# Kernel tuning notes

Measured on AMD Instinct MI355X. Metric: run time of the kernel, lower is better.

## Reference

```python
import jax, jax.numpy as jnp
import numpy as np

V, E, H, B, T, O = 100000, 300, 512, 512, 64, 2


def setup_inputs() -> dict:
    key = jax.random.key(0)
    ks = jax.random.split(key, 12)
    bound = 1.0 / np.sqrt(H)
    u = lambda k, shape: jax.random.uniform(k, shape, jnp.float32, -bound, bound)
    tokens = jax.random.randint(ks[0], (B, T), 0, V)  # int token ids
    emb = jax.random.normal(ks[1], (V, E), jnp.float32) * 0.05  # pretrained embeddings
    # GRU params stacked over 2 directions: [2, 3H, in], [2, 3H, H], [2, 3H]
    w_ih0 = u(ks[2], (2, 3 * H, E))
    w_hh0 = u(ks[3], (2, 3 * H, H))
    b_ih0 = u(ks[4], (2, 3 * H))
    b_hh0 = u(ks[5], (2, 3 * H))
    w_ih1 = u(ks[6], (2, 3 * H, 2 * H))
    w_hh1 = u(ks[7], (2, 3 * H, H))
    b_ih1 = u(ks[8], (2, 3 * H))
    b_hh1 = u(ks[9], (2, 3 * H))
    fc_w = u(ks[10], (O, 2 * H))
    fc_b = u(ks[11], (O,))
    return dict(tokens=tokens, emb=emb, w_ih0=w_ih0, w_hh0=w_hh0, b_ih0=b_ih0,
                b_hh0=b_hh0, w_ih1=w_ih1, w_hh1=w_hh1, b_ih1=b_ih1, b_hh1=b_hh1,
                fc_w=fc_w, fc_b=fc_b)


def _gru_dir(x, Wih, Whh, bih, bhh):
    # x: [B, T, in] -> [B, T, H]; PyTorch GRU cell math.
    gx = jnp.einsum('bti,gi->btg', x, Wih) + bih  # input gates precomputed [B,T,3H]
    h_units = Whh.shape[1]

    def step(h, g):
        gh = h @ Whh.T + bhh
        xr, xz, xn = jnp.split(g, 3, axis=-1)
        hr, hz, hn = jnp.split(gh, 3, axis=-1)
        r = jax.nn.sigmoid(xr + hr)
        z = jax.nn.sigmoid(xz + hz)
        n = jnp.tanh(xn + r * hn)
        h_new = (1.0 - z) * n + z * h
        return h_new, h_new

    h0 = jnp.zeros((x.shape[0], h_units), x.dtype)
    _, ys = jax.lax.scan(step, h0, jnp.swapaxes(gx, 0, 1))  # scan over time
    return jnp.swapaxes(ys, 0, 1)


def _gru_bidir(x, w_ih, w_hh, b_ih, b_hh):
    fwd = _gru_dir(x, w_ih[0], w_hh[0], b_ih[0], b_hh[0])
    bwd = _gru_dir(x[:, ::-1], w_ih[1], w_hh[1], b_ih[1], b_hh[1])[:, ::-1]
    return jnp.concatenate([fwd, bwd], axis=-1)  # [B, T, 2H]


def reference(tokens, emb, w_ih0, w_hh0, b_ih0, b_hh0, w_ih1, w_hh1, b_ih1,
              b_hh1, fc_w, fc_b):
    x = emb[tokens]                                   # [B, T, E]
    h1 = _gru_bidir(x, w_ih0, w_hh0, b_ih0, b_hh0)    # [B, T, 2H]
    h2 = _gru_bidir(h1, w_ih1, w_hh1, b_ih1, b_hh1)   # [B, T, 2H]
    # dropout output is discarded in the original forward (out = output[:, -1, :])
    last = h2[:, -1, :]                               # [B, 2H]
    return last @ fc_w.T + fc_b                       # [B, O]
```

## Files before the change

### kernel.cpp

```cpp
#include <hip/hip_runtime.h>
#include <stdint.h>


#define NTW 192
#define MTX 2048

typedef _Float16 half8 __attribute__((ext_vector_type(8)));
typedef _Float16 half4_t __attribute__((ext_vector_type(4)));
typedef float float4_t __attribute__((ext_vector_type(4)));

__device__ __forceinline__ void gl_lds16(const void* g, void* l) {
  __builtin_amdgcn_global_load_lds(
      (const __attribute__((address_space(1))) void*)g,
      (__attribute__((address_space(3))) void*)l, 16, 0, 0);
}

__device__ __forceinline__ float sigm_f(float x) { return 1.f / (1.f + __expf(-x)); }
__device__ __forceinline__ float tanh_f(float x) { return 1.f - 2.f / (__expf(2.f * x) + 1.f); }

__global__ void pack_b_kernel(const float* __restrict__ src, _Float16* __restrict__ dst,
                              int K, int KI) {
  int gid = blockIdx.x * 256 + threadIdx.x;
  int l = gid & 63, unit = gid >> 6;
  int nt = unit / KI, ks = unit - nt * KI;
  if (nt >= NTW) return;
  int row = nt * 16 + (l & 15);
  int col0 = ks * 32 + ((l >> 4) << 3);
  half8 v;
#pragma unroll
  for (int j = 0; j < 8; ++j) {
    int c = col0 + j;
    v[j] = (c < K) ? (_Float16)src[(long)row * K + c] : (_Float16)0.f;
  }
  *(half8*)(dst + (long)unit * 512 + l * 8) = v;
}

__global__ void gather_kernel(const int* __restrict__ tokens, const float* __restrict__ emb,
                              _Float16* __restrict__ x0) {
  int gid = blockIdx.x * 256 + threadIdx.x;
  int l = gid & 63, unit = gid >> 6;
  int mt = unit / 10, ks = unit - mt * 10;
  if (mt >= MTX) return;
  int row = mt * 16 + (l & 15);
  const float* e = emb + (long)tokens[row] * 300;
  int col0 = ks * 32 + ((l >> 4) << 3);
  half8 v;
#pragma unroll
  for (int j = 0; j < 8; ++j) {
    int c = col0 + j;
    v[j] = (c < 300) ? (_Float16)e[c] : (_Float16)0.f;
  }
  *(half8*)(x0 + (long)unit * 512 + l * 8) = v;
}

__global__ __launch_bounds__(256) void gemm_bt_kernel(
    const _Float16* __restrict__ A, const _Float16* __restrict__ Bw,
    const float* __restrict__ bias, _Float16* __restrict__ C, int KI) {
  __shared__ _Float16 As[8 * 512];
  __shared__ _Float16 Bs[8 * 512];
  const int bx = blockIdx.x, by = blockIdx.y;
  const int tid = threadIdx.x, w = tid >> 6, l = tid & 63;
  const int wm = w >> 1, wn = w & 1, ln = l & 15;
  const int mt0 = by * 8, nt0 = bx * 8;
  float4_t acc[4][4];
#pragma unroll
  for (int i = 0; i < 4; ++i)
#pragma unroll
    for (int j = 0; j < 4; ++j) acc[i][j] = 0.f;
  for (int it = 0; it < KI; ++it) {
    __syncthreads();
    gl_lds16(A + ((long)(mt0 + w) * KI + it) * 512 + l * 8, As + w * 512 + l * 8);
    gl_lds16(A + ((long)(mt0 + w + 4) * KI + it) * 512 + l * 8, As + (w + 4) * 512 + l * 8);
    gl_lds16(Bw + ((long)(nt0 + w) * KI + it) * 512 + l * 8, Bs + w * 512 + l * 8);
    gl_lds16(Bw + ((long)(nt0 + w + 4) * KI + it) * 512 + l * 8, Bs + (w + 4) * 512 + l * 8);
    __syncthreads();
    half8 af[4], bf[4];
#pragma unroll
    for (int i = 0; i < 4; ++i) af[i] = *(const half8*)(As + (wm * 4 + i) * 512 + l * 8);
#pragma unroll
    for (int j = 0; j < 4; ++j) bf[j] = *(const half8*)(Bs + (wn * 4 + j) * 512 + l * 8);
#pragma unroll
    for (int i = 0; i < 4; ++i)
#pragma unroll
      for (int j = 0; j < 4; ++j)
        acc[i][j] = __builtin_amdgcn_mfma_f32_16x16x32_f16(af[i], bf[j], acc[i][j], 0, 0, 0);
  }
#pragma unroll
  for (int i = 0; i < 4; ++i)
#pragma unroll
    for (int j = 0; j < 4; ++j) {
      int mt = mt0 + wm * 4 + i, ntile = nt0 + wn * 4 + j;
      float bv = bias[ntile * 16 + ln];
      half4_t o;
#pragma unroll
      for (int r = 0; r < 4; ++r) o[r] = (_Float16)(acc[i][j][r] + bv);
      *(half4_t*)(C + ((long)mt * NTW + ntile) * 256 + l * 4) = o;
    }
}

__global__ __launch_bounds__(256, 1) void gru_scan_kernel(
    const _Float16* __restrict__ whh,
    const float* __restrict__ bhh,
    const _Float16* __restrict__ gx,
    _Float16* hbuf, _Float16* ys,
    float* last,
    unsigned int* cnt) {
  __shared__ alignas(16) _Float16 hsA[16 * 512];
  __shared__ alignas(16) _Float16 hsB[16 * 512];
  __shared__ alignas(16) _Float16 hx[2 * 512];
  const int bid = blockIdx.x;
  const int d = bid >> 7, mp = (bid >> 3) & 15, ntb = bid & 7;
  const int rA = mp * 2, rB = rA + 1;
  const int tid = threadIdx.x, w = tid >> 6, l = tid & 63;
  const int lq = l >> 4, ln = l & 15;
  unsigned int* flagsA = cnt + (d * 32 + rA) * 16;
  unsigned int* flagsB = cnt + (d * 32 + rB) * 16;
  const int hcol = ntb * 64 + w * 16 + ln;

  half8 bf[3][16];
#pragma unroll
  for (int g = 0; g < 3; ++g) {
    const int tg = d * 96 + g * 32 + ntb * 4 + w;
#pragma unroll
    for (int ks = 0; ks < 16; ++ks)
      bf[g][ks] = *(const half8*)(whh + (long)(tg * 16 + ks) * 512 + l * 8);
  }
  const float bh0 = bhh[d * 1536 + hcol];
  const float bh1 = bhh[d * 1536 + 512 + hcol];
  const float bh2 = bhh[d * 1536 + 1024 + hcol];
  float hrA[4] = {0.f, 0.f, 0.f, 0.f};
  float hrB[4] = {0.f, 0.f, 0.f, 0.f};
  const int ntg0 = d * 96 + ntb * 4 + w;
  const unsigned long long* hb8 = (const unsigned long long*)hbuf;
  unsigned long long* hb8w = (unsigned long long*)hbuf;
  unsigned long long* lA64 = (unsigned long long*)hsA;
  unsigned long long* lB64 = (unsigned long long*)hsB;
  const unsigned long long* hx64 = (const unsigned long long*)hx;

  float xrA[4], xzA[4], xnA[4], xrB[4], xzB[4], xnB[4];
  auto load_gx = [&](int step, int rc, float (&vr)[4], float (&vz)[4], float (&vn)[4]) {
    const int t2 = d ? (63 - step) : step;
    const int rm2 = t2 & 15, tq2 = t2 >> 4;
    const int eoff2 = ((rm2 >> 2) * 16 + ln) * 4 + (rm2 & 3);
#pragma unroll
    for (int r = 0; r < 4; ++r) {
      const int b = rc * 16 + lq * 4 + r;
      const long gbase = ((long)(b * 4 + tq2) * 192 + ntg0) * 256 + eoff2;
      vr[r] = (float)gx[gbase];
      vz[r] = (float)gx[gbase + 32 * 256];
      vn[r] = (float)gx[gbase + 64 * 256];
    }
  };
  load_gx(0, rA, xrA, xzA, xnA);
  load_gx(0, rB, xrB, xzB, xnB);

  auto poll = [&](unsigned int* flags, unsigned int tgt) {
    long guard = 0;
    for (;;) {
      const unsigned int f = __hip_atomic_load(flags + (l & 7), __ATOMIC_RELAXED,
                                               __HIP_MEMORY_SCOPE_AGENT);
      if (__all((int)(f >= tgt))) break;
      __builtin_amdgcn_s_sleep(1);
      if (++guard > (1L << 24)) break;
    }
  };

  for (int s = 0; s < 64; ++s) {
    const int par = s & 1;
    const int t_in = d ? (63 - s) : s;
    const int rm = t_in & 15, tq = t_in >> 4;
    const unsigned long long* src = hb8 + (long)(d * 2 + par) * 65536;

    poll(flagsA, (unsigned int)s);
    poll(flagsB, (unsigned int)s);
    __builtin_amdgcn_fence(__ATOMIC_ACQUIRE, "workgroup");
    unsigned long long ta[8], tb[8];
#pragma unroll
    for (int j = 0; j < 8; ++j)
      ta[j] = __hip_atomic_load(src + (long)rA * 2048 + j * 256 + tid, __ATOMIC_RELAXED,
                                __HIP_MEMORY_SCOPE_AGENT);
#pragma unroll
    for (int j = 0; j < 8; ++j)
      tb[j] = __hip_atomic_load(src + (long)rB * 2048 + j * 256 + tid, __ATOMIC_RELAXED,
                                __HIP_MEMORY_SCOPE_AGENT);
#pragma unroll
    for (int j = 0; j < 8; ++j) lA64[j * 256 + tid] = ta[j];
    __syncthreads();

    float4_t accA[3];
    accA[0] = 0.f; accA[1] = 0.f; accA[2] = 0.f;
#pragma unroll
    for (int kk = 0; kk < 2; ++kk) {
      half8 af[8];
#pragma unroll
      for (int k2 = 0; k2 < 8; ++k2)
        af[k2] = *(const half8*)(hsA + (kk * 8 + k2) * 512 + l * 8);
#pragma unroll
      for (int k2 = 0; k2 < 8; ++k2)
#pragma unroll
        for (int g = 0; g < 3; ++g)
          accA[g] = __builtin_amdgcn_mfma_f32_16x16x32_f16(af[k2], bf[g][kk * 8 + k2],
                                                           accA[g], 0, 0, 0);
    }
#pragma unroll
    for (int j = 0; j < 8; ++j) lB64[j * 256 + tid] = tb[j];

#pragma unroll
    for (int r = 0; r < 4; ++r) {
      const int b = rA * 16 + lq * 4 + r;
      const long gmt = (long)b * 4 + tq;
      const float rg = sigm_f(xrA[r] + accA[0][r] + bh0);
      const float zg = sigm_f(xzA[r] + accA[1][r] + bh1);
      const float ng = tanh_f(xnA[r] + rg * (accA[2][r] + bh2));
      const float hv = (1.f - zg) * ng + zg * hrA[r];
      hrA[r] = hv;
      hx[(w >> 1) * 512 + (((w & 1) * 2 + (ln >> 3)) * 16 + lq * 4 + r) * 8 + (ln & 7)] =
          (_Float16)hv;
      if (ys != nullptr) {
        const int kcol = d * 512 + hcol;
        ys[(gmt * 32 + (kcol >> 5)) * 512 + (((kcol >> 3) & 3) * 16 + rm) * 8 + (kcol & 7)] =
            (_Float16)hv;
      }
      if (last != nullptr && ((d == 0 && s == 63) || (d == 1 && s == 0)))
        last[(long)b * 1024 + d * 512 + hcol] = hv;
    }
    __syncthreads();

    if (s < 63) {
      const unsigned long long qa = hx64[tid];
      unsigned long long* dst = hb8w + (long)(d * 2 + (par ^ 1)) * 65536 +
                                (long)rA * 2048 + (ntb * 2 + (tid >> 7)) * 128 + (tid & 127);
      __hip_atomic_store(dst, qa, __ATOMIC_RELAXED, __HIP_MEMORY_SCOPE_AGENT);
    }

    float4_t accB[3];
    accB[0] = 0.f; accB[1] = 0.f; accB[2] = 0.f;
#pragma unroll
    for (int kk = 0; kk < 2; ++kk) {
      half8 af[8];
#pragma unroll
      for (int k2 = 0; k2 < 8; ++k2)
        af[k2] = *(const half8*)(hsB + (kk * 8 + k2) * 512 + l * 8);
#pragma unroll
      for (int k2 = 0; k2 < 8; ++k2)
#pragma unroll
        for (int g = 0; g < 3; ++g)
          accB[g] = __builtin_amdgcn_mfma_f32_16x16x32_f16(af[k2], bf[g][kk * 8 + k2],
                                                           accB[g], 0, 0, 0);
    }
    __syncthreads();
    if (tid == 0 && s < 63)
      __hip_atomic_store(flagsA + ntb, (unsigned int)(s + 1), __ATOMIC_RELAXED,
                         __HIP_MEMORY_SCOPE_AGENT);

#pragma unroll
    for (int r = 0; r < 4; ++r) {
      const int b = rB * 16 + lq * 4 + r;
      const long gmt = (long)b * 4 + tq;
      const float rg = sigm_f(xrB[r] + accB[0][r] + bh0);
      const float zg = sigm_f(xzB[r] + accB[1][r] + bh1);
      const float ng = tanh_f(xnB[r] + rg * (accB[2][r] + bh2));
      const float hv = (1.f - zg) * ng + zg * hrB[r];
      hrB[r] = hv;
      hx[(w >> 1) * 512 + (((w & 1) * 2 + (ln >> 3)) * 16 + lq * 4 + r) * 8 + (ln & 7)] =
          (_Float16)hv;
      if (ys != nullptr) {
        const int kcol = d * 512 + hcol;
        ys[(gmt * 32 + (kcol >> 5)) * 512 + (((kcol >> 3) & 3) * 16 + rm) * 8 + (kcol & 7)] =
            (_Float16)hv;
      }
      if (last != nullptr && ((d == 0 && s == 63) || (d == 1 && s == 0)))
        last[(long)b * 1024 + d * 512 + hcol] = hv;
    }
    if (s == 63) break;

    __syncthreads();
    {
      const unsigned long long qb = hx64[tid];
      unsigned long long* dst = hb8w + (long)(d * 2 + (par ^ 1)) * 65536 +
                                (long)rB * 2048 + (ntb * 2 + (tid >> 7)) * 128 + (tid & 127);
      __hip_atomic_store(dst, qb, __ATOMIC_RELAXED, __HIP_MEMORY_SCOPE_AGENT);
    }
    __syncthreads();
    if (tid == 0)
      __hip_atomic_store(flagsB + ntb, (unsigned int)(s + 1), __ATOMIC_RELAXED,
                         __HIP_MEMORY_SCOPE_AGENT);

    load_gx(s + 1, rA, xrA, xzA, xnA);
    load_gx(s + 1, rB, xrB, xzB, xnB);
  }
}

__global__ void fc_kernel(const float* __restrict__ lastb, const float* __restrict__ fw,
                          const float* __restrict__ fb, float* __restrict__ out) {
  const int b = blockIdx.x, l = threadIdx.x;
  const float* x = lastb + (long)b * 1024;
  float a0 = 0.f, a1 = 0.f;
  for (int k = l; k < 1024; k += 64) {
    const float v = x[k];
    a0 += v * fw[k];
    a1 += v * fw[1024 + k];
  }
#pragma unroll
  for (int off = 32; off > 0; off >>= 1) {
    a0 += __shfl_down(a0, off, 64);
    a1 += __shfl_down(a1, off, 64);
  }
  if (l == 0) {
    out[b * 2 + 0] = a0 + fb[0];
    out[b * 2 + 1] = a1 + fb[1];
  }
}

extern "C" void kernel_launch(void* const* d_in, const int* in_sizes, int n_in,
                              void* d_out, int out_size, void* d_ws, size_t ws_size,
                              hipStream_t stream) {
  const int* tokens = (const int*)d_in[0];
  const float* emb = (const float*)d_in[1];
  const float* w_ih0 = (const float*)d_in[2];
  const float* w_hh0 = (const float*)d_in[3];
  const float* b_ih0 = (const float*)d_in[4];
  const float* b_hh0 = (const float*)d_in[5];
  const float* w_ih1 = (const float*)d_in[6];
  const float* w_hh1 = (const float*)d_in[7];
  const float* b_ih1 = (const float*)d_in[8];
  const float* b_hh1 = (const float*)d_in[9];
  const float* fc_w = (const float*)d_in[10];
  const float* fc_b = (const float*)d_in[11];
  float* out = (float*)d_out;

  char* ws = (char*)d_ws;
  size_t off = 0;
  auto alloc = [&](size_t bytes) -> void* {
    void* p = ws + off;
    off += (bytes + 255) & ~(size_t)255;
    return p;
  };
  _Float16* W0f = (_Float16*)alloc(192L * 10 * 512 * 2);
  _Float16* W1f = (_Float16*)alloc(192L * 32 * 512 * 2);
  _Float16* Wh0f = (_Float16*)alloc(192L * 16 * 512 * 2);
  _Float16* Wh1f = (_Float16*)alloc(192L * 16 * 512 * 2);
  _Float16* x0f = (_Float16*)alloc(2048L * 10 * 512 * 2);
  _Float16* x1f = (_Float16*)alloc(2048L * 32 * 512 * 2);
  _Float16* gxb = (_Float16*)alloc(2048L * 192 * 256 * 2);
  char* hz = ws + off;
  _Float16* hbuf = (_Float16*)alloc(4L * 32 * 8192 * 2);
  unsigned int* cnt = (unsigned int*)alloc(4096);
  const size_t hz_bytes = 4L * 32 * 8192 * 2 + 4096;
  float* lastb = (float*)alloc(512L * 1024 * 4);
  if (off > ws_size) return;

  pack_b_kernel<<<dim3(192 * 10 * 64 / 256), 256, 0, stream>>>(w_ih0, W0f, 300, 10);
  pack_b_kernel<<<dim3(192 * 32 * 64 / 256), 256, 0, stream>>>(w_ih1, W1f, 1024, 32);
  pack_b_kernel<<<dim3(192 * 16 * 64 / 256), 256, 0, stream>>>(w_hh0, Wh0f, 512, 16);
  pack_b_kernel<<<dim3(192 * 16 * 64 / 256), 256, 0, stream>>>(w_hh1, Wh1f, 512, 16);
  gather_kernel<<<dim3(2048 * 10 * 64 / 256), 256, 0, stream>>>(tokens, emb, x0f);

  gemm_bt_kernel<<<dim3(24, 256), 256, 0, stream>>>(x0f, W0f, b_ih0, gxb, 10);
  hipMemsetAsync(hz, 0, hz_bytes, stream);
  gru_scan_kernel<<<dim3(256), 256, 0, stream>>>(Wh0f, b_hh0, gxb, hbuf, x1f, nullptr, cnt);

  gemm_bt_kernel<<<dim3(24, 256), 256, 0, stream>>>(x1f, W1f, b_ih1, gxb, 32);
  hipMemsetAsync(hz, 0, hz_bytes, stream);
  gru_scan_kernel<<<dim3(256), 256, 0, stream>>>(Wh1f, b_hh1, gxb, hbuf, nullptr, lastb, cnt);

  fc_kernel<<<dim3(512), 64, 0, stream>>>(lastb, fc_w, fc_b, out);
}
```

Measured before the change: 1.218 ms.

## Replace flag counters with sentinel-valued per-step hidden-state slots for inter-block sync

The scan kernel stops publishing per-row flag counters and polling them before reading the hidden state. Instead each time step gets its own buffer slot, pre-filled with an all-ones sentinel, and consumers spin directly on the data until no word equals the sentinel. This removes the flag round trip and the extra barriers around flag stores. Row-B polling is also deferred until after the row-A MFMA work so the two waits can overlap. The cost is a much larger hidden-state buffer (64 slots per direction) that must be memset to the sentinel before each layer, adding memset traffic. It also assumes a real fp16 hidden-state word never equals the sentinel, and replaces __syncthreads with a hand-written lgkmcnt wait plus s_barrier.

Measured after the change: 1.398 ms. 1.15x slower.

```diff
diff --git a/kernel.cpp b/kernel.cpp
--- a/kernel.cpp
+++ b/kernel.cpp
@@ -17,6 +17,12 @@
 
 __device__ __forceinline__ float sigm_f(float x) { return 1.f / (1.f + __expf(-x)); }
 __device__ __forceinline__ float tanh_f(float x) { return 1.f - 2.f / (__expf(2.f * x) + 1.f); }
+
+__device__ __forceinline__ void ldsbar() {
+  asm volatile("s_waitcnt lgkmcnt(0)" ::: "memory");
+  __builtin_amdgcn_sched_barrier(0);
+  __builtin_amdgcn_s_barrier();
+}
 
 __global__ void pack_b_kernel(const float* __restrict__ src, _Float16* __restrict__ dst,
                               int K, int KI) {
@@ -103,8 +109,7 @@
     const float* __restrict__ bhh,
     const _Float16* __restrict__ gx,
     _Float16* hbuf, _Float16* ys,
-    float* last,
-    unsigned int* cnt) {
+    float* last) {
   __shared__ alignas(16) _Float16 hsA[16 * 512];
   __shared__ alignas(16) _Float16 hsB[16 * 512];
   __shared__ alignas(16) _Float16 hx[2 * 512];
@@ -113,8 +118,6 @@
   const int rA = mp * 2, rB = rA + 1;
   const int tid = threadIdx.x, w = tid >> 6, l = tid & 63;
   const int lq = l >> 4, ln = l & 15;
-  unsigned int* flagsA = cnt + (d * 32 + rA) * 16;
-  unsigned int* flagsB = cnt + (d * 32 + rB) * 16;
   const int hcol = ntb * 64 + w * 16 + ln;
 
   half8 bf[3][16];
@@ -136,6 +139,7 @@
   unsigned long long* lA64 = (unsigned long long*)hsA;
   unsigned long long* lB64 = (unsigned long long*)hsB;
   const unsigned long long* hx64 = (const unsigned long long*)hx;
+  const unsigned long long SENT = ~0ULL;
 
   float xrA[4], xzA[4], xnA[4], xrB[4], xzB[4], xnB[4];
   auto load_gx = [&](int step, int rc, float (&vr)[4], float (&vz)[4], float (&vn)[4]) {
@@ -154,38 +158,33 @@
   load_gx(0, rA, xrA, xzA, xnA);
   load_gx(0, rB, xrB, xzB, xnB);
 
-  auto poll = [&](unsigned int* flags, unsigned int tgt) {
-    long guard = 0;
-    for (;;) {
-      const unsigned int f = __hip_atomic_load(flags + (l & 7), __ATOMIC_RELAXED,
-                                               __HIP_MEMORY_SCOPE_AGENT);
-      if (__all((int)(f >= tgt))) break;
-      __builtin_amdgcn_s_sleep(1);
-      if (++guard > (1L << 24)) break;
+  auto poll8 = [&](const unsigned long long* src, unsigned long long (&t)[8]) {
+#pragma unroll
+    for (int j = 0; j < 8; ++j)
+      t[j] = __hip_atomic_load(src + j * 256 + tid, __ATOMIC_RELAXED,
+                               __HIP_MEMORY_SCOPE_AGENT);
+#pragma unroll
+    for (int j = 0; j < 8; ++j) {
+      long guard = 0;
+      while (t[j] == SENT) {
+        __builtin_amdgcn_s_sleep(1);
+        t[j] = __hip_atomic_load(src + j * 256 + tid, __ATOMIC_RELAXED,
+                                 __HIP_MEMORY_SCOPE_AGENT);
+        if (++guard > (1L << 24)) break;
+      }
     }
   };
 
   for (int s = 0; s < 64; ++s) {
-    const int par = s & 1;
     const int t_in = d ? (63 - s) : s;
     const int rm = t_in & 15, tq = t_in >> 4;
-    const unsigned long long* src = hb8 + (long)(d * 2 + par) * 65536;
-
-    poll(flagsA, (unsigned int)s);
-    poll(flagsB, (unsigned int)s);
-    __builtin_amdgcn_fence(__ATOMIC_ACQUIRE, "workgroup");
-    unsigned long long ta[8], tb[8];
-#pragma unroll
-    for (int j = 0; j < 8; ++j)
-      ta[j] = __hip_atomic_load(src + (long)rA * 2048 + j * 256 + tid, __ATOMIC_RELAXED,
-                                __HIP_MEMORY_SCOPE_AGENT);
-#pragma unroll
-    for (int j = 0; j < 8; ++j)
-      tb[j] = __hip_atomic_load(src + (long)rB * 2048 + j * 256 + tid, __ATOMIC_RELAXED,
-                                __HIP_MEMORY_SCOPE_AGENT);
+    const unsigned long long* slot = hb8 + (long)(d * 64 + s) * 65536;
+
+    unsigned long long ta[8];
+    poll8(slot + (long)rA * 2048, ta);
 #pragma unroll
     for (int j = 0; j < 8; ++j) lA64[j * 256 + tid] = ta[j];
-    __syncthreads();
+    ldsbar();
 
     float4_t accA[3];
     accA[0] = 0.f; accA[1] = 0.f; accA[2] = 0.f;
@@ -202,6 +201,9 @@
           accA[g] = __builtin_amdgcn_mfma_f32_16x16x32_f16(af[k2], bf[g][kk * 8 + k2],
                                                            accA[g], 0, 0, 0);
     }
+
+    unsigned long long tb[8];
+    poll8(slot + (long)rB * 2048, tb);
 #pragma unroll
     for (int j = 0; j < 8; ++j) lB64[j * 256 + tid] = tb[j];
 
@@ -224,11 +226,11 @@
       if (last != nullptr && ((d == 0 && s == 63) || (d == 1 && s == 0)))
         last[(long)b * 1024 + d * 512 + hcol] = hv;
     }
-    __syncthreads();
+    ldsbar();
 
     if (s < 63) {
       const unsigned long long qa = hx64[tid];
-      unsigned long long* dst = hb8w + (long)(d * 2 + (par ^ 1)) * 65536 +
+      unsigned long long* dst = hb8w + (long)(d * 64 + s + 1) * 65536 +
                                 (long)rA * 2048 + (ntb * 2 + (tid >> 7)) * 128 + (tid & 127);
       __hip_atomic_store(dst, qa, __ATOMIC_RELAXED, __HIP_MEMORY_SCOPE_AGENT);
     }
@@ -248,10 +250,7 @@
           accB[g] = __builtin_amdgcn_mfma_f32_16x16x32_f16(af[k2], bf[g][kk * 8 + k2],
                                                            accB[g], 0, 0, 0);
     }
-    __syncthreads();
-    if (tid == 0 && s < 63)
-      __hip_atomic_store(flagsA + ntb, (unsigned int)(s + 1), __ATOMIC_RELAXED,
-                         __HIP_MEMORY_SCOPE_AGENT);
+    ldsbar();
 
 #pragma unroll
     for (int r = 0; r < 4; ++r) {
@@ -274,17 +273,13 @@
     }
     if (s == 63) break;
 
-    __syncthreads();
+    ldsbar();
     {
       const unsigned long long qb = hx64[tid];
-      unsigned long long* dst = hb8w + (long)(d * 2 + (par ^ 1)) * 65536 +
+      unsigned long long* dst = hb8w + (long)(d * 64 + s + 1) * 65536 +
                                 (long)rB * 2048 + (ntb * 2 + (tid >> 7)) * 128 + (tid & 127);
       __hip_atomic_store(dst, qb, __ATOMIC_RELAXED, __HIP_MEMORY_SCOPE_AGENT);
     }
-    __syncthreads();
-    if (tid == 0)
-      __hip_atomic_store(flagsB + ntb, (unsigned int)(s + 1), __ATOMIC_RELAXED,
-                         __HIP_MEMORY_SCOPE_AGENT);
 
     load_gx(s + 1, rA, xrA, xzA, xnA);
     load_gx(s + 1, rB, xrB, xzB, xnB);
@@ -336,6 +331,7 @@
     off += (bytes + 255) & ~(size_t)255;
     return p;
   };
+  const size_t HSLOT = 65536UL * 8;
   _Float16* W0f = (_Float16*)alloc(192L * 10 * 512 * 2);
   _Float16* W1f = (_Float16*)alloc(192L * 32 * 512 * 2);
   _Float16* Wh0f = (_Float16*)alloc(192L * 16 * 512 * 2);
@@ -343,10 +339,7 @@
   _Float16* x0f = (_Float16*)alloc(2048L * 10 * 512 * 2);
   _Float16* x1f = (_Float16*)alloc(2048L * 32 * 512 * 2);
   _Float16* gxb = (_Float16*)alloc(2048L * 192 * 256 * 2);
-  char* hz = ws + off;
-  _Float16* hbuf = (_Float16*)alloc(4L * 32 * 8192 * 2);
-  unsigned int* cnt = (unsigned int*)alloc(4096);
-  const size_t hz_bytes = 4L * 32 * 8192 * 2 + 4096;
+  _Float16* hbuf = (_Float16*)alloc(128UL * HSLOT);
   float* lastb = (float*)alloc(512L * 1024 * 4);
   if (off > ws_size) return;
 
@@ -357,12 +350,16 @@
   gather_kernel<<<dim3(2048 * 10 * 64 / 256), 256, 0, stream>>>(tokens, emb, x0f);
 
   gemm_bt_kernel<<<dim3(24, 256), 256, 0, stream>>>(x0f, W0f, b_ih0, gxb, 10);
-  hipMemsetAsync(hz, 0, hz_bytes, stream);
-  gru_scan_kernel<<<dim3(256), 256, 0, stream>>>(Wh0f, b_hh0, gxb, hbuf, x1f, nullptr, cnt);
+  hipMemsetAsync(hbuf, 0xFF, 128UL * HSLOT, stream);
+  hipMemsetAsync((char*)hbuf, 0, HSLOT, stream);
+  hipMemsetAsync((char*)hbuf + 64UL * HSLOT, 0, HSLOT, stream);
+  gru_scan_kernel<<<dim3(256), 256, 0, stream>>>(Wh0f, b_hh0, gxb, hbuf, x1f, nullptr);
 
   gemm_bt_kernel<<<dim3(24, 256), 256, 0, stream>>>(x1f, W1f, b_ih1, gxb, 32);
-  hipMemsetAsync(hz, 0, hz_bytes, stream);
-  gru_scan_kernel<<<dim3(256), 256, 0, stream>>>(Wh1f, b_hh1, gxb, hbuf, nullptr, lastb, cnt);
+  hipMemsetAsync(hbuf, 0xFF, 128UL * HSLOT, stream);
+  hipMemsetAsync((char*)hbuf, 0, HSLOT, stream);
+  hipMemsetAsync((char*)hbuf + 64UL * HSLOT, 0, HSLOT, stream);
+  gru_scan_kernel<<<dim3(256), 256, 0, stream>>>(Wh1f, b_hh1, gxb, hbuf, nullptr, lastb);
 
   fc_kernel<<<dim3(512), 64, 0, stream>>>(lastb, fc_w, fc_b, out);
 }
```

## Reorder GEMM rows time-major and lay out gate precompute for vector loads in scan

Applied to the files above, without the earlier changes.

Changes the row ordering of the token gather and layer inputs to time-major (t*512+b), and rewrites the GEMM output layout so each scan step reads its input-gate values as contiguous half4 vectors indexed by timestep and gate column. This replaces twelve scattered scalar fp16 loads per step with six vector loads issued alongside the hidden-state loads. It also merges the two flag polls into a single loop, double-buffers the hx staging arrays, and replaces __syncthreads with an LDS-only waitcnt plus barrier with scheduling fences. The cost is a different workspace layout that every producer and consumer must agree on, and reliance on hand-placed waits for correctness.

Result: slower. 1.255 ms (+3.0%).

```diff
diff --git a/kernel.cpp b/kernel.cpp
--- a/kernel.cpp
+++ b/kernel.cpp
@@ -17,6 +17,12 @@
 
 __device__ __forceinline__ float sigm_f(float x) { return 1.f / (1.f + __expf(-x)); }
 __device__ __forceinline__ float tanh_f(float x) { return 1.f - 2.f / (__expf(2.f * x) + 1.f); }
+
+__device__ __forceinline__ void ldsbar() {
+  asm volatile("s_waitcnt lgkmcnt(0)" ::: "memory");
+  __builtin_amdgcn_sched_barrier(0);
+  __builtin_amdgcn_s_barrier();
+}
 
 __global__ void pack_b_kernel(const float* __restrict__ src, _Float16* __restrict__ dst,
                               int K, int KI) {
@@ -42,7 +48,8 @@
   int mt = unit / 10, ks = unit - mt * 10;
   if (mt >= MTX) return;
   int row = mt * 16 + (l & 15);
-  const float* e = emb + (long)tokens[row] * 300;
+  int b = row & 511, t = row >> 9;
+  const float* e = emb + (long)tokens[b * 64 + t] * 300;
   int col0 = ks * 32 + ((l >> 4) << 3);
   half8 v;
 #pragma unroll
@@ -60,7 +67,7 @@
   __shared__ _Float16 Bs[8 * 512];
   const int bx = blockIdx.x, by = blockIdx.y;
   const int tid = threadIdx.x, w = tid >> 6, l = tid & 63;
-  const int wm = w >> 1, wn = w & 1, ln = l & 15;
+  const int wm = w >> 1, wn = w & 1, ln = l & 15, lq = l >> 4;
   const int mt0 = by * 8, nt0 = bx * 8;
   float4_t acc[4][4];
 #pragma unroll
@@ -94,7 +101,8 @@
       half4_t o;
 #pragma unroll
       for (int r = 0; r < 4; ++r) o[r] = (_Float16)(acc[i][j][r] + bv);
-      *(half4_t*)(C + ((long)mt * NTW + ntile) * 256 + l * 4) = o;
+      *(half4_t*)(C + ((long)(mt >> 5) * 3072 + ntile * 16 + ln) * 512 +
+                  (mt & 31) * 16 + lq * 4) = o;
     }
 }
 
@@ -107,7 +115,8 @@
     unsigned int* cnt) {
   __shared__ alignas(16) _Float16 hsA[16 * 512];
   __shared__ alignas(16) _Float16 hsB[16 * 512];
-  __shared__ alignas(16) _Float16 hx[2 * 512];
+  __shared__ alignas(16) _Float16 hxA[1024];
+  __shared__ alignas(16) _Float16 hxB[1024];
   const int bid = blockIdx.x;
   const int d = bid >> 7, mp = (bid >> 3) & 15, ntb = bid & 7;
   const int rA = mp * 2, rB = rA + 1;
@@ -130,50 +139,34 @@
   const float bh2 = bhh[d * 1536 + 1024 + hcol];
   float hrA[4] = {0.f, 0.f, 0.f, 0.f};
   float hrB[4] = {0.f, 0.f, 0.f, 0.f};
-  const int ntg0 = d * 96 + ntb * 4 + w;
   const unsigned long long* hb8 = (const unsigned long long*)hbuf;
   unsigned long long* hb8w = (unsigned long long*)hbuf;
   unsigned long long* lA64 = (unsigned long long*)hsA;
   unsigned long long* lB64 = (unsigned long long*)hsB;
-  const unsigned long long* hx64 = (const unsigned long long*)hx;
-
-  float xrA[4], xzA[4], xnA[4], xrB[4], xzB[4], xnB[4];
-  auto load_gx = [&](int step, int rc, float (&vr)[4], float (&vz)[4], float (&vn)[4]) {
-    const int t2 = d ? (63 - step) : step;
-    const int rm2 = t2 & 15, tq2 = t2 >> 4;
-    const int eoff2 = ((rm2 >> 2) * 16 + ln) * 4 + (rm2 & 3);
-#pragma unroll
-    for (int r = 0; r < 4; ++r) {
-      const int b = rc * 16 + lq * 4 + r;
-      const long gbase = ((long)(b * 4 + tq2) * 192 + ntg0) * 256 + eoff2;
-      vr[r] = (float)gx[gbase];
-      vz[r] = (float)gx[gbase + 32 * 256];
-      vn[r] = (float)gx[gbase + 64 * 256];
-    }
-  };
-  load_gx(0, rA, xrA, xzA, xnA);
-  load_gx(0, rB, xrB, xzB, xnB);
-
-  auto poll = [&](unsigned int* flags, unsigned int tgt) {
-    long guard = 0;
-    for (;;) {
-      const unsigned int f = __hip_atomic_load(flags + (l & 7), __ATOMIC_RELAXED,
-                                               __HIP_MEMORY_SCOPE_AGENT);
-      if (__all((int)(f >= tgt))) break;
-      __builtin_amdgcn_s_sleep(1);
-      if (++guard > (1L << 24)) break;
-    }
-  };
+  const unsigned long long* hxA64 = (const unsigned long long*)hxA;
+  const unsigned long long* hxB64 = (const unsigned long long*)hxB;
 
   for (int s = 0; s < 64; ++s) {
     const int par = s & 1;
     const int t_in = d ? (63 - s) : s;
-    const int rm = t_in & 15, tq = t_in >> 4;
     const unsigned long long* src = hb8 + (long)(d * 2 + par) * 65536;
 
-    poll(flagsA, (unsigned int)s);
-    poll(flagsB, (unsigned int)s);
+    {
+      const unsigned int tgt = (unsigned int)s;
+      long guard = 0;
+      for (;;) {
+        const unsigned int fa = __hip_atomic_load(flagsA + (l & 7), __ATOMIC_RELAXED,
+                                                  __HIP_MEMORY_SCOPE_AGENT);
+        const unsigned int fb = __hip_atomic_load(flagsB + (l & 7), __ATOMIC_RELAXED,
+                                                  __HIP_MEMORY_SCOPE_AGENT);
+        if (__all((int)(fa >= tgt && fb >= tgt))) break;
+        __builtin_amdgcn_s_sleep(1);
+        if (++guard > (1L << 24)) break;
+      }
+    }
     __builtin_amdgcn_fence(__ATOMIC_ACQUIRE, "workgroup");
+    __builtin_amdgcn_sched_barrier(0);
+
     unsigned long long ta[8], tb[8];
 #pragma unroll
     for (int j = 0; j < 8; ++j)
@@ -183,9 +176,26 @@
     for (int j = 0; j < 8; ++j)
       tb[j] = __hip_atomic_load(src + (long)rB * 2048 + j * 256 + tid, __ATOMIC_RELAXED,
                                 __HIP_MEMORY_SCOPE_AGENT);
+    __builtin_amdgcn_sched_barrier(0);
+
+    half4_t gA[3], gB[3];
+    {
+      const long gb = ((long)t_in * 3072 + d * 1536 + hcol) * 512;
+      const int bA = rA * 16 + lq * 4, bB = rB * 16 + lq * 4;
+      gA[0] = *(const half4_t*)(gx + gb + bA);
+      gA[1] = *(const half4_t*)(gx + gb + 512L * 512 + bA);
+      gA[2] = *(const half4_t*)(gx + gb + 1024L * 512 + bA);
+      gB[0] = *(const half4_t*)(gx + gb + bB);
+      gB[1] = *(const half4_t*)(gx + gb + 512L * 512 + bB);
+      gB[2] = *(const half4_t*)(gx + gb + 1024L * 512 + bB);
+    }
+    __builtin_amdgcn_sched_barrier(0);
+
 #pragma unroll
     for (int j = 0; j < 8; ++j) lA64[j * 256 + tid] = ta[j];
-    __syncthreads();
+#pragma unroll
+    for (int j = 0; j < 8; ++j) lB64[j * 256 + tid] = tb[j];
+    ldsbar();
 
     float4_t accA[3];
     accA[0] = 0.f; accA[1] = 0.f; accA[2] = 0.f;
@@ -202,32 +212,29 @@
           accA[g] = __builtin_amdgcn_mfma_f32_16x16x32_f16(af[k2], bf[g][kk * 8 + k2],
                                                            accA[g], 0, 0, 0);
     }
-#pragma unroll
-    for (int j = 0; j < 8; ++j) lB64[j * 256 + tid] = tb[j];
 
 #pragma unroll
     for (int r = 0; r < 4; ++r) {
       const int b = rA * 16 + lq * 4 + r;
-      const long gmt = (long)b * 4 + tq;
-      const float rg = sigm_f(xrA[r] + accA[0][r] + bh0);
-      const float zg = sigm_f(xzA[r] + accA[1][r] + bh1);
-      const float ng = tanh_f(xnA[r] + rg * (accA[2][r] + bh2));
+      const float rg = sigm_f((float)gA[0][r] + accA[0][r] + bh0);
+      const float zg = sigm_f((float)gA[1][r] + accA[1][r] + bh1);
+      const float ng = tanh_f((float)gA[2][r] + rg * (accA[2][r] + bh2));
       const float hv = (1.f - zg) * ng + zg * hrA[r];
       hrA[r] = hv;
-      hx[(w >> 1) * 512 + (((w & 1) * 2 + (ln >> 3)) * 16 + lq * 4 + r) * 8 + (ln & 7)] =
+      hxA[(w >> 1) * 512 + (((w & 1) * 2 + (ln >> 3)) * 16 + lq * 4 + r) * 8 + (ln & 7)] =
           (_Float16)hv;
       if (ys != nullptr) {
         const int kcol = d * 512 + hcol;
-        ys[(gmt * 32 + (kcol >> 5)) * 512 + (((kcol >> 3) & 3) * 16 + rm) * 8 + (kcol & 7)] =
-            (_Float16)hv;
+        ys[((long)(t_in * 32 + rA) * 32 + (kcol >> 5)) * 512 +
+           (((kcol >> 3) & 3) * 16 + lq * 4 + r) * 8 + (kcol & 7)] = (_Float16)hv;
       }
       if (last != nullptr && ((d == 0 && s == 63) || (d == 1 && s == 0)))
         last[(long)b * 1024 + d * 512 + hcol] = hv;
     }
-    __syncthreads();
+    ldsbar();
 
     if (s < 63) {
-      const unsigned long long qa = hx64[tid];
+      const unsigned long long qa = hxA64[tid];
       unsigned long long* dst = hb8w + (long)(d * 2 + (par ^ 1)) * 65536 +
                                 (long)rA * 2048 + (ntb * 2 + (tid >> 7)) * 128 + (tid & 127);
       __hip_atomic_store(dst, qa, __ATOMIC_RELAXED, __HIP_MEMORY_SCOPE_AGENT);
@@ -256,27 +263,26 @@
 #pragma unroll
     for (int r = 0; r < 4; ++r) {
       const int b = rB * 16 + lq * 4 + r;
-      const long gmt = (long)b * 4 + tq;
-      const float rg = sigm_f(xrB[r] + accB[0][r] + bh0);
-      const float zg = sigm_f(xzB[r] + accB[1][r] + bh1);
-      const float ng = tanh_f(xnB[r] + rg * (accB[2][r] + bh2));
+      const float rg = sigm_f((float)gB[0][r] + accB[0][r] + bh0);
+      const float zg = sigm_f((float)gB[1][r] + accB[1][r] + bh1);
+      const float ng = tanh_f((float)gB[2][r] + rg * (accB[2][r] + bh2));
       const float hv = (1.f - zg) * ng + zg * hrB[r];
       hrB[r] = hv;
-      hx[(w >> 1) * 512 + (((w & 1) * 2 + (ln >> 3)) * 16 + lq * 4 + r) * 8 + (ln & 7)] =
+      hxB[(w >> 1) * 512 + (((w & 1) * 2 + (ln >> 3)) * 16 + lq * 4 + r) * 8 + (ln & 7)] =
           (_Float16)hv;
       if (ys != nullptr) {
         const int kcol = d * 512 + hcol;
-        ys[(gmt * 32 + (kcol >> 5)) * 512 + (((kcol >> 3) & 3) * 16 + rm) * 8 + (kcol & 7)] =
-            (_Float16)hv;
+        ys[((long)(t_in * 32 + rB) * 32 + (kcol >> 5)) * 512 +
+           (((kcol >> 3) & 3) * 16 + lq * 4 + r) * 8 + (kcol & 7)] = (_Float16)hv;
       }
       if (last != nullptr && ((d == 0 && s == 63) || (d == 1 && s == 0)))
         last[(long)b * 1024 + d * 512 + hcol] = hv;
     }
     if (s == 63) break;
 
-    __syncthreads();
+    ldsbar();
     {
-      const unsigned long long qb = hx64[tid];
+      const unsigned long long qb = hxB64[tid];
       unsigned long long* dst = hb8w + (long)(d * 2 + (par ^ 1)) * 65536 +
                                 (long)rB * 2048 + (ntb * 2 + (tid >> 7)) * 128 + (tid & 127);
       __hip_atomic_store(dst, qb, __ATOMIC_RELAXED, __HIP_MEMORY_SCOPE_AGENT);
@@ -285,9 +291,6 @@
     if (tid == 0)
       __hip_atomic_store(flagsB + ntb, (unsigned int)(s + 1), __ATOMIC_RELAXED,
                          __HIP_MEMORY_SCOPE_AGENT);
-
-    load_gx(s + 1, rA, xrA, xzA, xnA);
-    load_gx(s + 1, rB, xrB, xzB, xnB);
   }
 }
 
@@ -342,7 +345,7 @@
   _Float16* Wh1f = (_Float16*)alloc(192L * 16 * 512 * 2);
   _Float16* x0f = (_Float16*)alloc(2048L * 10 * 512 * 2);
   _Float16* x1f = (_Float16*)alloc(2048L * 32 * 512 * 2);
-  _Float16* gxb = (_Float16*)alloc(2048L * 192 * 256 * 2);
+  _Float16* gxb = (_Float16*)alloc(64L * 3072 * 512 * 2);
   char* hz = ws + off;
   _Float16* hbuf = (_Float16*)alloc(4L * 32 * 8192 * 2);
   unsigned int* cnt = (unsigned int*)alloc(4096);
```
